# Kernel optimization log

Measured on AMD Instinct MI355X. Metric: run time of the kernel, lower is better.

## Reference

```python
import jax, jax.numpy as jnp
import numpy as np
from jax import lax

HEADS = 4
DSTATE = 8
DHALF = 64
DTRANK = 8
GRID_SIZE = 5
SPLINE_ORDER = 3


def _ln(x, g, b, eps=1e-5):
    mu = x.mean(-1, keepdims=True)
    v = ((x - mu) ** 2).mean(-1, keepdims=True)
    return (x - mu) / jnp.sqrt(v + eps) * g + b


def _make_grid(in_f):
    h = 2.0 / GRID_SIZE
    g = jnp.arange(-SPLINE_ORDER, GRID_SIZE + SPLINE_ORDER + 1, dtype=jnp.float32) * h - 1.0
    return jnp.tile(g[None, :], (in_f, 1))  # (in, grid+2k+1)


def _b_splines(x, grid):
    # x: (batch, in); grid: (in, G+2k+1) -> (batch, in, G+k)
    xe = x[:, :, None]
    bases = ((xe >= grid[:, :-1]) & (xe < grid[:, 1:])).astype(x.dtype)
    for k in range(1, SPLINE_ORDER + 1):
        bases = ((xe - grid[:, :-(k + 1)]) / (grid[:, k:-1] - grid[:, :-(k + 1)])) * bases[:, :, :-1] \
              + ((grid[:, k + 1:] - xe) / (grid[:, k + 1:] - grid[:, 1:-k])) * bases[:, :, 1:]
    return bases


def _kan_layer(x, bw, sw, sc, grid):
    base = jax.nn.silu(x) @ bw.T
    bs = _b_splines(x, grid)
    return base + jnp.einsum('bic,oic->bo', bs, sw * sc[:, :, None])


def _fkan(x, ng, nb, bw0, sw0, sc0, bw1, sw1, sc1):
    B, N, C = x.shape
    xf = _ln(x, ng, nb).reshape(B * N, C)
    h = _kan_layer(xf, bw0, sw0, sc0, _make_grid(C))
    y = _kan_layer(h, bw1, sw1, sc1, _make_grid(bw0.shape[0]))
    return y.reshape(B, N, C)


def _conv1x1(x, w, b):
    return jnp.einsum('bchw,oc->bohw', x, w[:, :, 0, 0]) + b[None, :, None, None]


def _dwconv2d(x, w, b):
    y = lax.conv_general_dilated(x, w, (1, 1), 'SAME', feature_group_count=x.shape[1],
                                 dimension_numbers=('NCHW', 'OIHW', 'NCHW'))
    return y + b[None, :, None, None]


def _dwconv1d(x, w):
    return lax.conv_general_dilated(x, w, (1,), 'SAME', feature_group_count=x.shape[1],
                                    dimension_numbers=('NCH', 'OIH', 'NCH'))


def _attention(x, temp, qkv_w, qkv_b, dw_w, dw_b, po_w, po_b):
    b, c, h, w = x.shape
    qkv = _dwconv2d(_conv1x1(x, qkv_w, qkv_b), dw_w, dw_b)
    q, k, v = jnp.split(qkv, 3, axis=1)
    rs = lambda t: t.reshape(b, HEADS, c // HEADS, h * w)
    q, k, v = rs(q), rs(k), rs(v)
    q = q / jnp.maximum(jnp.linalg.norm(q, axis=-1, keepdims=True), 1e-12)
    k = k / jnp.maximum(jnp.linalg.norm(k, axis=-1, keepdims=True), 1e-12)
    attn = jax.nn.softmax(jnp.einsum('bhcn,bhdn->bhcd', q, k) * temp, axis=-1)
    out = jnp.einsum('bhcd,bhdn->bhcn', attn, v).reshape(b, c, h, w)
    return _conv1x1(out, po_w, po_b)


def _mamba(x, in_w, xp_w, dt_w, dt_b, A_log, Dp, out_w, cx_w, cz_w):
    B, L, C = x.shape
    xz = x @ in_w.T                       # (B, L, d_inner)
    xc, zc = jnp.split(xz, 2, axis=-1)    # each (B, L, DHALF)
    xl = jax.nn.silu(_dwconv1d(xc.transpose(0, 2, 1), cx_w)).transpose(0, 2, 1)
    zl = jax.nn.silu(_dwconv1d(zc.transpose(0, 2, 1), cz_w)).transpose(0, 2, 1)
    x_dbl = xl @ xp_w.T                   # (B, L, dt_rank + 2*d_state)
    dt, Bm, Cm = jnp.split(x_dbl, [DTRANK, DTRANK + DSTATE], axis=-1)
    delta = jax.nn.softplus(dt @ dt_w.T + dt_b)   # (B, L, DHALF)
    A = -jnp.exp(A_log)                   # (DHALF, DSTATE)
    dA = jnp.exp(jnp.einsum('bld,dn->bldn', delta, A))
    dBu = delta[..., None] * Bm[:, :, None, :] * xl[..., None]

    def step(hst, inp):
        dA_t, dBu_t, C_t = inp
        hst = dA_t * hst + dBu_t
        return hst, jnp.einsum('bdn,bn->bd', hst, C_t)

    h0 = jnp.zeros((B, DHALF, DSTATE), x.dtype)
    _, ys = lax.scan(step, h0, (dA.transpose(1, 0, 2, 3), dBu.transpose(1, 0, 2, 3), Cm.transpose(1, 0, 2)))
    y = ys.transpose(1, 0, 2) + xl * Dp
    return jnp.concatenate([y, zl], axis=-1) @ out_w.T


def _forward(x5d, ln1_g, ln1_b, ln2_g, ln2_b, ln3_g, ln3_b, ln4_g, ln4_b,
             attn_temp, attn_qkv_w, attn_qkv_b, attn_dw_w, attn_dw_b, attn_po_w, attn_po_b,
             ffn1_ng, ffn1_nb, ffn1_bw0, ffn1_sw0, ffn1_sc0, ffn1_bw1, ffn1_sw1, ffn1_sc1,
             ffn2_ng, ffn2_nb, ffn2_bw0, ffn2_sw0, ffn2_sc0, ffn2_bw1, ffn2_sw1, ffn2_sc1,
             in_proj_w, x_proj_w, dt_proj_w, dt_proj_b, A_log, D_param, out_proj_w, conv_x_w, conv_z_w):
    B, C, Dd, H, W = x5d.shape
    N = Dd * H * W
    Hs = int(np.sqrt(N))
    x = x5d.reshape(B, C, N).transpose(0, 2, 1)   # (B, N, C)
    t2d = _ln(x, ln1_g, ln1_b).transpose(0, 2, 1).reshape(B, C, Hs, Hs)
    a = _attention(t2d, attn_temp, attn_qkv_w, attn_qkv_b, attn_dw_w, attn_dw_b, attn_po_w, attn_po_b)
    t = x + a.reshape(B, C, N).transpose(0, 2, 1)
    u = _fkan(_ln(t, ln2_g, ln2_b), ffn1_ng, ffn1_nb, ffn1_bw0, ffn1_sw0, ffn1_sc0, ffn1_bw1, ffn1_sw1, ffn1_sc1) + t
    x_tr = x + u
    m = _mamba(_ln(x_tr, ln3_g, ln3_b), in_proj_w, x_proj_w, dt_proj_w, dt_proj_b, A_log, D_param, out_proj_w, conv_x_w, conv_z_w) + x_tr
    n = _fkan(_ln(m, ln4_g, ln4_b), ffn2_ng, ffn2_nb, ffn2_bw0, ffn2_sw0, ffn2_sc0, ffn2_bw1, ffn2_sw1, ffn2_sc1) + m
    out = x_tr + n
    return out.transpose(0, 2, 1).reshape(B, C, Dd, H, W)


def setup_inputs():
    key = jax.random.key(0)
    ks = iter(jax.random.split(key, 48))
    f32 = jnp.float32

    def rn(shape, s=0.05):
        return jax.random.normal(next(ks), shape, f32) * s

    B, C, Dd, H, W = 2, 128, 1, 96, 96
    MLP = 512
    d = {}
    d['x5d'] = jax.random.normal(next(ks), (B, C, Dd, H, W), f32)
    for nm in ('ln1', 'ln2', 'ln3', 'ln4'):
        d[nm + '_g'] = jnp.ones((C,), f32)
        d[nm + '_b'] = jnp.zeros((C,), f32)
    d['attn_temp'] = jnp.ones((HEADS, 1, 1), f32)
    d['attn_qkv_w'] = rn((3 * C, C, 1, 1)); d['attn_qkv_b'] = jnp.zeros((3 * C,), f32)
    d['attn_dw_w'] = rn((3 * C, 1, 3, 3), 0.2); d['attn_dw_b'] = jnp.zeros((3 * C,), f32)
    d['attn_po_w'] = rn((C, C, 1, 1)); d['attn_po_b'] = jnp.zeros((C,), f32)
    for p in ('ffn1', 'ffn2'):
        d[p + '_ng'] = jnp.ones((C,), f32); d[p + '_nb'] = jnp.zeros((C,), f32)
        d[p + '_bw0'] = rn((MLP, C)); d[p + '_sw0'] = rn((MLP, C, GRID_SIZE + SPLINE_ORDER), 0.02); d[p + '_sc0'] = jnp.ones((MLP, C), f32)
        d[p + '_bw1'] = rn((C, MLP)); d[p + '_sw1'] = rn((C, MLP, GRID_SIZE + SPLINE_ORDER), 0.02); d[p + '_sc1'] = jnp.ones((C, MLP), f32)
    d['in_proj_w'] = rn((C, C))
    d['x_proj_w'] = rn((DTRANK + 2 * DSTATE, DHALF))
    std = DTRANK ** -0.5
    d['dt_proj_w'] = jax.random.uniform(next(ks), (DHALF, DTRANK), f32, -std, std)
    dt = jnp.exp(jax.random.uniform(next(ks), (DHALF,), f32) * (np.log(0.1) - np.log(0.001)) + np.log(0.001))
    dt = jnp.clip(dt, 1e-4, None)
    d['dt_proj_b'] = dt + jnp.log(-jnp.expm1(-dt))
    d['A_log'] = jnp.log(jnp.tile(jnp.arange(1, DSTATE + 1, dtype=f32)[None, :], (DHALF, 1)))
    d['D_param'] = jnp.ones((DHALF,), f32)
    d['out_proj_w'] = rn((C, C))
    d['conv_x_w'] = rn((DHALF, 1, 3), 0.2)
    d['conv_z_w'] = rn((DHALF, 1, 3), 0.2)
    return d


def reference(x5d, ln1_g, ln1_b, ln2_g, ln2_b, ln3_g, ln3_b, ln4_g, ln4_b,
              attn_temp, attn_qkv_w, attn_qkv_b, attn_dw_w, attn_dw_b, attn_po_w, attn_po_b,
              ffn1_ng, ffn1_nb, ffn1_bw0, ffn1_sw0, ffn1_sc0, ffn1_bw1, ffn1_sw1, ffn1_sc1,
              ffn2_ng, ffn2_nb, ffn2_bw0, ffn2_sw0, ffn2_sc0, ffn2_bw1, ffn2_sw1, ffn2_sc1,
              in_proj_w, x_proj_w, dt_proj_w, dt_proj_b, A_log, D_param, out_proj_w, conv_x_w, conv_z_w):
    return _forward(x5d, ln1_g, ln1_b, ln2_g, ln2_b, ln3_g, ln3_b, ln4_g, ln4_b,
                    attn_temp, attn_qkv_w, attn_qkv_b, attn_dw_w, attn_dw_b, attn_po_w, attn_po_b,
                    ffn1_ng, ffn1_nb, ffn1_bw0, ffn1_sw0, ffn1_sc0, ffn1_bw1, ffn1_sw1, ffn1_sc1,
                    ffn2_ng, ffn2_nb, ffn2_bw0, ffn2_sw0, ffn2_sc0, ffn2_bw1, ffn2_sw1, ffn2_sc1,
                    in_proj_w, x_proj_w, dt_proj_w, dt_proj_b, A_log, D_param, out_proj_w, conv_x_w, conv_z_w)
```

## Files before the change

### kernel.cpp

```cpp
#include <hip/hip_runtime.h>

typedef unsigned short u16;
typedef __attribute__((ext_vector_type(8))) short bh8;
typedef __attribute__((ext_vector_type(4))) float f4;

#define DI __device__ __forceinline__

DI u16 f2bf(float f){ unsigned u=__float_as_uint(f); u += 0x7fffu + ((u>>16)&1u); return (u16)(u>>16); }
DI float bf2f(u16 u){ return __uint_as_float(((unsigned)u)<<16); }
DI float silu_f(float x){ return x/(1.f+__expf(-x)); }

DI void gld16(const u16* g, u16* l){
  __builtin_amdgcn_global_load_lds((const __attribute__((address_space(1))) void*)g,
                                   (__attribute__((address_space(3))) void*)l, 16, 0, 0);
}

DI void bspline8(float x, float* v){
  float u = x*2.5f + 5.5f;
  #pragma unroll
  for (int j=0;j<8;j++){
    float a  = fabsf(u - (float)(j+2));
    float t1 = fmaxf(2.f-a, 0.f);
    float t2 = fmaxf(1.f-a, 0.f);
    v[j] = t1*t1*t1*(1.f/6.f) - t2*t2*t2*(2.f/3.f);
  }
}

template<int KAN_H, bool OUT_BF16>
__global__ __launch_bounds__(256, 6)
void gemm64(const void* __restrict__ Asrc, const u16* __restrict__ Bt,
            void* __restrict__ Cout, int M, int N, int K, int ktiles_per_z,
            int split, const float* __restrict__ bias, const float* __restrict__ R1)
{
  __shared__ __align__(128) u16 smem[12296];
  u16* const sB = smem;
  u16* const sA = smem + 8192;
  const int m0 = blockIdx.y * 64;
  const int n0 = blockIdx.x * 128;
  const int ktiles = K >> 6;
  int kt0 = blockIdx.z * ktiles_per_z;
  int kt1 = kt0 + ktiles_per_z; if (kt1 > ktiles) kt1 = ktiles;
  const int t = threadIdx.x;
  const int wave = t >> 6, lane = t & 63;
  const int lr = lane & 15, lq = lane >> 4;
  const int lr8 = lane >> 3, lc8 = lane & 7;
  const int swz8 = lc8 ^ lr8;
  f4 acc[4][2];
  f4 z4 = {0.f,0.f,0.f,0.f};
  #pragma unroll
  for (int i=0;i<4;i++){ acc[i][0]=z4; acc[i][1]=z4; }

  for (int kt = kt0; kt < kt1; ++kt) {
    int k0 = kt << 6;
    {
      const u16* Bp = Bt + (size_t)n0 * K + k0;
      #pragma unroll
      for (int it=0; it<4; ++it) {
        int r = it*32 + wave*8;
        gld16(Bp + (size_t)(r + lr8) * K + swz8*8, &sB[r*64]);
      }
    }
    if (KAN_H == 0) {
      const u16* Ap = (const u16*)Asrc + (size_t)m0 * K + k0;
      #pragma unroll
      for (int it=0; it<2; ++it) {
        int r = it*32 + wave*8;
        gld16(Ap + (size_t)(r + lr8) * K + swz8*8, &sA[r*64]);
      }
    } else {
      const u16* hsrc = (const u16*)Asrc;
      if (k0 < KAN_H) {
        #pragma unroll
        for (int it=0; it<2; ++it) {
          int chunk = t + it*256;
          int r = chunk >> 3, ck = chunk & 7;
          const u16* src = hsrc + (size_t)(m0+r)*KAN_H + k0 + ck*8;
          ushort4 a = *(const ushort4*)src;
          ushort4 b2 = *(const ushort4*)(src+4);
          alignas(16) u16 o[8];
          o[0]=f2bf(silu_f(bf2f(a.x))); o[1]=f2bf(silu_f(bf2f(a.y)));
          o[2]=f2bf(silu_f(bf2f(a.z))); o[3]=f2bf(silu_f(bf2f(a.w)));
          o[4]=f2bf(silu_f(bf2f(b2.x))); o[5]=f2bf(silu_f(bf2f(b2.y)));
          o[6]=f2bf(silu_f(bf2f(b2.z))); o[7]=f2bf(silu_f(bf2f(b2.w)));
          *(float4*)(&sA[r*64 + (ck ^ (r&7))*8]) = *(const float4*)o;
        }
      } else {
        int i0 = (k0 - KAN_H) >> 3;
        const float4 zf4 = make_float4(0.f,0.f,0.f,0.f);
        #pragma unroll
        for (int it=0; it<2; ++it) {
          int pair = t + it*256;
          int r = pair >> 3, ii = pair & 7;
          int base = r*64 + (ii ^ (r&7))*8;
          *(float4*)(&sA[base]) = zf4;
          float x = bf2f(hsrc[(size_t)(m0+r)*KAN_H + i0 + ii]);
          float u = x*2.5f + 5.5f;
          bool valid = (u >= 0.f) & (u < 11.f);
          float uc = fminf(fmaxf(u, 0.f), 10.999f);
          int m = (int)uc;
          float tt = uc - (float)m;
          float omt = 1.f - tt, t2 = tt*tt, t3 = t2*tt;
          float w0 = omt*omt*omt*(1.f/6.f);
          float w3 = t3*(1.f/6.f);
          float w1 = 0.5f*t3 - t2 + (2.f/3.f);
          float w2 = 1.f - w0 - w1 - w3;
          float ws[4] = {w0, w1, w2, w3};
          int c0 = m - 3;
          #pragma unroll
          for (int j=0;j<4;j++){
            int c = c0 + j;
            bool ok = valid & ((unsigned)c < 8u);
            int off = ok ? (base + c) : 4096;
            sA[off] = f2bf(ws[j]);
          }
        }
      }
    }
    __syncthreads();
    #pragma unroll
    for (int kk=0; kk<64; kk+=32) {
      const int c0k = kk >> 3;
      bh8 af[4], bfr[2];
      #pragma unroll
      for (int i=0;i<4;i++) {
        int row = i*16 + lr;
        af[i] = *(const bh8*)(&sA[row*64 + ((c0k+lq) ^ (row&7))*8]);
      }
      #pragma unroll
      for (int j=0;j<2;j++) {
        int row = wave*32 + j*16 + lr;
        bfr[j] = *(const bh8*)(&sB[row*64 + ((c0k+lq) ^ (row&7))*8]);
      }
      #pragma unroll
      for (int i=0;i<4;i++)
        #pragma unroll
        for (int j=0;j<2;j++)
          acc[i][j] = __builtin_amdgcn_mfma_f32_16x16x32_bf16(af[i], bfr[j], acc[i][j], 0, 0, 0);
    }
    __syncthreads();
  }
  if (OUT_BF16) {
    u16* Cb = (u16*)Cout;
    #pragma unroll
    for (int i=0;i<4;i++) {
      #pragma unroll
      for (int j=0;j<2;j++) {
        int col = wave*32 + j*16 + lr;
        float bv = bias ? bias[n0 + col] : 0.f;
        #pragma unroll
        for (int r4=0;r4<4;r4++) {
          int row = i*16 + lq*4 + r4;
          smem[row*136 + col] = f2bf(acc[i][j][r4] + bv);
        }
      }
    }
    __syncthreads();
    #pragma unroll
    for (int it=0; it<4; ++it) {
      int idx = t + it*256;
      int row = idx >> 4, seg = idx & 15;
      *(float4*)(Cb + (size_t)(m0+row)*N + n0 + seg*8) =
          *(const float4*)&smem[row*136 + seg*8];
    }
  } else {
    float* Cf = (float*)Cout;
    if (split) Cf += (size_t)blockIdx.z * M * N;
    #pragma unroll
    for (int i=0;i<4;i++) {
      int row = m0 + i*16 + lq*4;
      #pragma unroll
      for (int j=0;j<2;j++) {
        int col = n0 + wave*32 + j*16 + lr;
        float bv = bias ? bias[col] : 0.f;
        #pragma unroll
        for (int r4=0;r4<4;r4++) {
          size_t idx = (size_t)(row + r4) * N + col;
          float v = acc[i][j][r4] + bv;
          if (R1) v += R1[idx];
          Cf[idx] = v;
        }
      }
    }
  }
}

__global__ __launch_bounds__(256) void k_ln1_trans(const float* __restrict__ x5d,
    float* __restrict__ x_t, u16* __restrict__ ln1_t,
    const float* __restrict__ g, const float* __restrict__ bv)
{
  __shared__ float tile[128*65];
  __shared__ float red_s[256], red_q[256];
  __shared__ float st_mu[64], st_rs[64];
  int b = blockIdx.y, n0 = blockIdx.x * 64;
  int j = threadIdx.x & 63, part = threadIdx.x >> 6;
  for (int cc=0; cc<32; ++cc) {
    int c = part*32 + cc;
    tile[c*65 + j] = x5d[((size_t)b*128 + c)*9216 + n0 + j];
  }
  __syncthreads();
  float s=0.f, s2=0.f;
  for (int cc=0; cc<32; ++cc) {
    float v = tile[(part*32+cc)*65 + j];
    s += v; s2 += v*v;
  }
  red_s[threadIdx.x]=s; red_q[threadIdx.x]=s2;
  __syncthreads();
  if (threadIdx.x < 64) {
    int jj = threadIdx.x;
    float ts = red_s[jj]+red_s[jj+64]+red_s[jj+128]+red_s[jj+192];
    float tq = red_q[jj]+red_q[jj+64]+red_q[jj+128]+red_q[jj+192];
    float mu = ts*(1.f/128.f);
    st_mu[jj]=mu;
    st_rs[jj]=rsqrtf(tq*(1.f/128.f) - mu*mu + 1e-5f);
  }
  __syncthreads();
  for (int it=0; it<32; ++it) {
    int idx = threadIdx.x + it*256;
    int tok = idx >> 7, c = idx & 127;
    float v = tile[c*65 + tok];
    size_t a = ((size_t)b*9216 + n0 + tok)*128 + c;
    x_t[a] = v;
    ln1_t[a] = f2bf((v - st_mu[tok])*st_rs[tok]*g[c] + bv[c]);
  }
}

__global__ void k_ln_double_expand(const float* __restrict__ in, u16* __restrict__ A1,
    const float* __restrict__ g1, const float* __restrict__ b1,
    const float* __restrict__ g2, const float* __restrict__ b2)
{
  int tok = blockIdx.x*4 + (threadIdx.x>>6);
  int lane = threadIdx.x & 63;
  const float* row = in + (size_t)tok*128;
  float v0=row[lane], v1=row[lane+64];
  float s=v0+v1, s2=v0*v0+v1*v1;
  #pragma unroll
  for (int o=1;o<64;o<<=1){ s += __shfl_xor(s,o); s2 += __shfl_xor(s2,o); }
  float mu=s*(1.f/128.f);
  float rs=rsqrtf(s2*(1.f/128.f)-mu*mu+1e-5f);
  float y0=(v0-mu)*rs*g1[lane]+b1[lane];
  float y1=(v1-mu)*rs*g1[lane+64]+b1[lane+64];
  s=y0+y1; s2=y0*y0+y1*y1;
  #pragma unroll
  for (int o=1;o<64;o<<=1){ s += __shfl_xor(s,o); s2 += __shfl_xor(s2,o); }
  mu=s*(1.f/128.f);
  rs=rsqrtf(s2*(1.f/128.f)-mu*mu+1e-5f);
  y0=(y0-mu)*rs*g2[lane]+b2[lane];
  y1=(y1-mu)*rs*g2[lane+64]+b2[lane+64];
  u16* arow = A1 + (size_t)tok*1152;
  arow[lane]    = f2bf(silu_f(y0));
  arow[lane+64] = f2bf(silu_f(y1));
  float w[8]; alignas(16) u16 o8[8];
  bspline8(y0, w);
  #pragma unroll
  for (int j=0;j<8;j++) o8[j]=f2bf(w[j]);
  *(float4*)(&arow[128 + lane*8]) = *(const float4*)o8;
  bspline8(y1, w);
  #pragma unroll
  for (int j=0;j<8;j++) o8[j]=f2bf(w[j]);
  *(float4*)(&arow[128 + (lane+64)*8]) = *(const float4*)o8;
}

__global__ __launch_bounds__(256) void k_dwconv(const u16* __restrict__ qkv_t,
    u16* __restrict__ qkvd, const float* __restrict__ dw_w, const float* __restrict__ dw_b)
{
  __shared__ float lt[100*68];
  int tile = blockIdx.x; int th=(tile/12)*8, tw=(tile%12)*8;
  int cg = blockIdx.y, b = blockIdx.z;
  int t = threadIdx.x;
  for (int pp=0; pp<7; ++pp) {
    int pos = pp*16 + (t>>4);
    if (pos < 100) {
      int ih = th + pos/10 - 1, iw = tw + pos%10 - 1;
      int c4 = (t & 15)*4;
      float4 v = make_float4(0.f,0.f,0.f,0.f);
      if (ih>=0 && ih<96 && iw>=0 && iw<96) {
        ushort4 raw = *(const ushort4*)&qkv_t[(((size_t)b*9216) + ih*96 + iw)*384 + cg*64 + c4];
        v = make_float4(bf2f(raw.x), bf2f(raw.y), bf2f(raw.z), bf2f(raw.w));
      }
      *(float4*)&lt[pos*68 + c4] = v;
    }
  }
  __syncthreads();
  int ch = t & 63, gch = cg*64 + ch;
  float w[9];
  #pragma unroll
  for (int k=0;k<9;k++) w[k]=dw_w[gch*9+k];
  float bias = dw_b[gch];
  for (int pp=0; pp<16; ++pp) {
    int pos = (t>>6) + pp*4;
    int oh = pos>>3, ow = pos&7;
    float acc = bias;
    #pragma unroll
    for (int di=0; di<3; ++di)
      #pragma unroll
      for (int dj=0; dj<3; ++dj)
        acc += lt[((oh+di)*10 + ow+dj)*68 + ch] * w[di*3+dj];
    qkvd[(((size_t)b*9216) + (th+oh)*96 + tw+ow)*384 + gch] = f2bf(acc);
  }
}

__global__ void k_normsum(const u16* __restrict__ qkvd, float* __restrict__ ss)
{
  int b = blockIdx.y, n0 = blockIdx.x*128;
  int c = threadIdx.x;
  float acc=0.f;
  for (int i=0;i<128;++i){
    float v = bf2f(qkvd[((size_t)b*9216 + n0+i)*384 + c]);
    acc += v*v;
  }
  atomicAdd(&ss[b*256 + c], acc);
}

__global__ __launch_bounds__(256) void k_qk(const u16* __restrict__ qkvd,
    const float* __restrict__ ss, float* __restrict__ S)
{
  __shared__ float ql[128][32];
  __shared__ float kl[128][32];
  int nc=blockIdx.x, h=blockIdx.y, b=blockIdx.z;
  int t = threadIdx.x;
  int r = t>>1, half = t&1;
  size_t rowa = ((size_t)b*9216 + nc*128 + r)*384 + (half?128:0) + h*32;
  #pragma unroll
  for (int cc=0; cc<32; ++cc) {
    float v = bf2f(qkvd[rowa + cc]);
    if (half) kl[r][cc]=v; else ql[r][cc]=v;
  }
  __syncthreads();
  int i0 = (t>>4)*2, j0 = (t&15)*2;
  float a00=0.f,a01=0.f,a10=0.f,a11=0.f;
  for (int n=0;n<128;++n){
    float2 qv = *(const float2*)&ql[n][i0];
    float2 kv = *(const float2*)&kl[n][j0];
    a00 += qv.x*kv.x; a01 += qv.x*kv.y;
    a10 += qv.y*kv.x; a11 += qv.y*kv.y;
  }
  const float* ssb = ss + b*256;
  float rq0 = 1.f/fmaxf(sqrtf(ssb[h*32+i0]),1e-12f);
  float rq1 = 1.f/fmaxf(sqrtf(ssb[h*32+i0+1]),1e-12f);
  float rk0 = 1.f/fmaxf(sqrtf(ssb[128+h*32+j0]),1e-12f);
  float rk1 = 1.f/fmaxf(sqrtf(ssb[128+h*32+j0+1]),1e-12f);
  float* Sp = S + ((size_t)(b*4+h))*1024;
  atomicAdd(&Sp[i0*32+j0],     a00*rq0*rk0);
  atomicAdd(&Sp[i0*32+j0+1],   a01*rq0*rk1);
  atomicAdd(&Sp[(i0+1)*32+j0], a10*rq1*rk0);
  atomicAdd(&Sp[(i0+1)*32+j0+1], a11*rq1*rk1);
}

__global__ void k_softmax(const float* __restrict__ S, float* __restrict__ attnP,
                          const float* __restrict__ temp)
{
  int bh = blockIdx.x; int h = bh & 3;
  int i = threadIdx.x;
  const float* row = S + (size_t)bh*1024 + i*32;
  float tp = temp[h];
  float vals[32]; float mx = -1e30f;
  #pragma unroll
  for (int j=0;j<32;++j){ float v=row[j]*tp; vals[j]=v; mx=fmaxf(mx,v); }
  float sum=0.f;
  #pragma unroll
  for (int j=0;j<32;++j){ vals[j]=__expf(vals[j]-mx); sum+=vals[j]; }
  float inv=1.f/sum;
  float* out = attnP + (size_t)bh*1024 + i*32;
  #pragma unroll
  for (int j=0;j<32;++j) out[j]=vals[j]*inv;
}

__global__ __launch_bounds__(256) void k_av(const u16* __restrict__ qkvd,
    const float* __restrict__ attnP, u16* __restrict__ attnout)
{
  __shared__ float at[1024];
  int b=blockIdx.z, h=blockIdx.y;
  int n = blockIdx.x*256 + threadIdx.x;
  #pragma unroll
  for (int it=0;it<4;++it)
    at[threadIdx.x + it*256] = attnP[((size_t)(b*4+h))*1024 + threadIdx.x + it*256];
  __syncthreads();
  const u16* vrow = &qkvd[((size_t)b*9216 + n)*384 + 256 + h*32];
  float acc[32];
  #pragma unroll
  for (int i=0;i<32;++i) acc[i]=0.f;
  #pragma unroll 4
  for (int j=0;j<32;++j){
    float vj = bf2f(vrow[j]);
    #pragma unroll
    for (int i=0;i<32;++i) acc[i] += at[i*32+j]*vj;
  }
  u16* orow = &attnout[((size_t)b*9216 + n)*128 + h*32];
  #pragma unroll
  for (int i=0;i<32;++i) orow[i] = f2bf(acc[i]);
}

__global__ void k_reduce4(const float4* __restrict__ P, const float4* __restrict__ R1,
                          const float4* __restrict__ R2, float4* __restrict__ o, int n4)
{
  int i = blockIdx.x*256 + threadIdx.x;
  if (i<n4){
    float4 a=P[i], b=P[i+n4], c=P[i+2*n4], d=P[i+3*n4], r=R1[i], s=R2[i];
    o[i]=make_float4(a.x+b.x+c.x+d.x+r.x+s.x, a.y+b.y+c.y+d.y+r.y+s.y,
                     a.z+b.z+c.z+d.z+r.z+s.z, a.w+b.w+c.w+d.w+r.w+s.w);
  }
}

__global__ void k_reduce4_ln(const float4* __restrict__ P, const float4* __restrict__ R1,
    const float4* __restrict__ R2, float4* __restrict__ xtr, u16* __restrict__ xm,
    const float* __restrict__ g, const float* __restrict__ bv, int n4)
{
  int i = blockIdx.x*256 + threadIdx.x;
  int q = i & 31;
  float4 a=P[i], b=P[i+n4], c=P[i+2*n4], d=P[i+3*n4], r=R1[i], s=R2[i];
  float4 v=make_float4(a.x+b.x+c.x+d.x+r.x+s.x, a.y+b.y+c.y+d.y+r.y+s.y,
                       a.z+b.z+c.z+d.z+r.z+s.z, a.w+b.w+c.w+d.w+r.w+s.w);
  xtr[i]=v;
  float s1 = v.x+v.y+v.z+v.w;
  float s2 = v.x*v.x+v.y*v.y+v.z*v.z+v.w*v.w;
  #pragma unroll
  for (int o=1;o<32;o<<=1){ s1 += __shfl_xor(s1,o); s2 += __shfl_xor(s2,o); }
  float mu = s1*(1.f/128.f);
  float rs = rsqrtf(s2*(1.f/128.f)-mu*mu+1e-5f);
  float4 g4 = *(const float4*)(g + q*4);
  float4 b4 = *(const float4*)(bv + q*4);
  ushort4 o4;
  o4.x = f2bf((v.x-mu)*rs*g4.x + b4.x);
  o4.y = f2bf((v.y-mu)*rs*g4.y + b4.y);
  o4.z = f2bf((v.z-mu)*rs*g4.z + b4.z);
  o4.w = f2bf((v.w-mu)*rs*g4.w + b4.w);
  ((ushort4*)xm)[i] = o4;
}

__global__ void k_prep(const float* __restrict__ qkv_w, const float* __restrict__ po_w,
    const float* __restrict__ in_w, const float* __restrict__ out_w,
    const float* __restrict__ A_log, u16* __restrict__ qkvw_bf, u16* __restrict__ pow_bf,
    u16* __restrict__ inw_bf, u16* __restrict__ outw_bf, float* __restrict__ Aneg,
    float* __restrict__ zbuf, int nz)
{
  int i = blockIdx.x*256 + threadIdx.x;
  if (i < 49152) { qkvw_bf[i] = f2bf(qkv_w[i]); return; }
  i -= 49152;
  if (i < 16384) { pow_bf[i] = f2bf(po_w[i]); return; }
  i -= 16384;
  if (i < 16384) { inw_bf[i] = f2bf(in_w[i]); return; }
  i -= 16384;
  if (i < 16384) { outw_bf[i] = f2bf(out_w[i]); return; }
  i -= 16384;
  if (i < 512) { Aneg[i] = -__expf(A_log[i]); return; }
  i -= 512;
  if (i < nz) zbuf[i] = 0.f;
}

__global__ __launch_bounds__(256) void k_mamba_pre(const float* __restrict__ xz,
    float* __restrict__ xl, float* __restrict__ delta,
    float* __restrict__ Bm, float* __restrict__ Cm, u16* __restrict__ A_out,
    const float* __restrict__ cxw, const float* __restrict__ czw,
    const float* __restrict__ xpw, const float* __restrict__ dtw, const float* __restrict__ dtb)
{
  __shared__ float xls[4][64];
  __shared__ float xds[4][24];
  int w = threadIdx.x>>6;
  int tok = blockIdx.x*4 + w;
  int lane = threadIdx.x & 63;
  int l = tok % 9216;
  size_t base = (size_t)tok*128;
  float xm1 = (l>0)?     xz[base-128+lane]    : 0.f;
  float x0  =            xz[base+lane];
  float xp1 = (l<9215)?  xz[base+128+lane]    : 0.f;
  float zm1 = (l>0)?     xz[base-128+64+lane] : 0.f;
  float z0  =            xz[base+64+lane];
  float zp1 = (l<9215)?  xz[base+128+64+lane] : 0.f;
  float xc = silu_f(cxw[lane*3]*xm1 + cxw[lane*3+1]*x0 + cxw[lane*3+2]*xp1);
  float zc = silu_f(czw[lane*3]*zm1 + czw[lane*3+1]*z0 + czw[lane*3+2]*zp1);
  xl[(size_t)tok*64+lane] = xc;
  A_out[(size_t)tok*128 + 64 + lane] = f2bf(zc);
  xls[w][lane] = xc;
  __syncthreads();
  if (lane < 24) {
    float s=0.f;
    #pragma unroll 8
    for (int c=0;c<64;++c) s += xls[w][c]*xpw[lane*64+c];
    xds[w][lane]=s;
  }
  __syncthreads();
  float dacc = dtb[lane];
  #pragma unroll
  for (int r=0;r<8;++r) dacc += xds[w][r]*dtw[lane*8+r];
  delta[(size_t)tok*64+lane] = (dacc>20.f)? dacc : log1pf(__expf(dacc));
  if (lane<8)       Bm[(size_t)tok*8+lane]   = xds[w][8+lane];
  else if (lane<16) Cm[(size_t)tok*8+lane-8] = xds[w][16+lane-8];
}

__global__ __launch_bounds__(512) void k_scan1(const float* __restrict__ delta,
    const float* __restrict__ Bm, const float* __restrict__ xl,
    const float* __restrict__ Aneg, float* __restrict__ cP, float* __restrict__ cS)
{
  int b=blockIdx.y, ch=blockIdx.x;
  int t=threadIdx.x; int d=t>>3, n=t&7;
  float An = Aneg[d*8+n];
  float P=1.f, S=0.f;
  int l0 = ch*96;
  #pragma unroll 8
  for (int i=0;i<96;++i){
    size_t s = (size_t)b*9216 + l0+i;
    float del = delta[s*64+d];
    float a = __expf(del*An);
    float dbu = del * Bm[s*8+n] * xl[s*64+d];
    P *= a; S = fmaf(a,S,dbu);
  }
  size_t o = ((size_t)(b*96+ch))*512 + t;
  cP[o]=P; cS[o]=S;
}

__global__ __launch_bounds__(512) void k_scan2(const float* __restrict__ cP,
    const float* __restrict__ cS, float* __restrict__ cI)
{
  int b=blockIdx.x; int t=threadIdx.x;
  float carry=0.f;
  #pragma unroll 4
  for (int c=0;c<96;++c){
    size_t o = ((size_t)(b*96+c))*512 + t;
    cI[o]=carry;
    carry = fmaf(cP[o], carry, cS[o]);
  }
}

__global__ __launch_bounds__(512) void k_scan3(const float* __restrict__ delta,
    const float* __restrict__ Bm, const float* __restrict__ Cm,
    const float* __restrict__ xl, const float* __restrict__ Aneg,
    const float* __restrict__ Dp, const float* __restrict__ cI, u16* __restrict__ A_out)
{
  int b=blockIdx.y, ch=blockIdx.x;
  int t=threadIdx.x; int d=t>>3, n=t&7;
  float An = Aneg[d*8+n];
  float h = cI[((size_t)(b*96+ch))*512 + t];
  float Dd = Dp[d];
  int l0 = ch*96;
  #pragma unroll 4
  for (int i=0;i<96;++i){
    size_t s = (size_t)b*9216 + l0+i;
    float del = delta[s*64+d];
    float a = __expf(del*An);
    float xv = xl[s*64+d];
    h = fmaf(a, h, del * Bm[s*8+n] * xv);
    float contrib = h * Cm[s*8+n];
    contrib += __shfl_xor(contrib,1);
    contrib += __shfl_xor(contrib,2);
    contrib += __shfl_xor(contrib,4);
    if (n==0) A_out[s*128 + d] = f2bf(contrib + xv*Dd);
  }
}

__global__ __launch_bounds__(256) void k_transpose_out(const float* __restrict__ sfin,
                                                       float* __restrict__ out)
{
  __shared__ float tile[128*65];
  int b=blockIdx.y, n0=blockIdx.x*64;
  for (int it=0;it<32;++it){
    int idx = threadIdx.x + it*256;
    int tok = idx>>7, c = idx&127;
    tile[c*65+tok] = sfin[((size_t)b*9216 + n0+tok)*128 + c];
  }
  __syncthreads();
  int j = threadIdx.x & 63, part = threadIdx.x>>6;
  for (int cc=0;cc<32;++cc){
    int c = part*32+cc;
    out[((size_t)b*128 + c)*9216 + n0 + j] = tile[c*65 + j];
  }
}

__global__ void k_pack_w1t(const float* __restrict__ bw0, const float* __restrict__ sw0,
                           const float* __restrict__ sc0, u16* __restrict__ W1t)
{
  int idx = blockIdx.x*256 + threadIdx.x;
  if (idx >= 512*1152) return;
  int o = idx/1152, k = idx%1152;
  float v;
  if (k < 128) v = bw0[o*128+k];
  else { int i=(k-128)>>3, c=(k-128)&7; v = sw0[(o*128+i)*8+c]*sc0[o*128+i]; }
  W1t[idx]=f2bf(v);
}
__global__ void k_pack_w2t(const float* __restrict__ bw1, const float* __restrict__ sw1,
                           const float* __restrict__ sc1, u16* __restrict__ W2t)
{
  int idx = blockIdx.x*256 + threadIdx.x;
  if (idx >= 128*4608) return;
  int o = idx/4608, k = idx%4608;
  float v;
  if (k < 512) v = bw1[o*512+k];
  else { int i=(k-512)>>3, c=(k-512)&7; v = sw1[(o*512+i)*8+c]*sc1[o*512+i]; }
  W2t[idx]=f2bf(v);
}

extern "C" void kernel_launch(void* const* d_in, const int* in_sizes, int n_in,
                              void* d_out, int out_size, void* d_ws, size_t ws_size,
                              hipStream_t stream)
{
  (void)in_sizes; (void)n_in; (void)out_size; (void)ws_size;
  const float* x5d   =(const float*)d_in[0];
  const float* ln1_g =(const float*)d_in[1];
  const float* ln1_b =(const float*)d_in[2];
  const float* ln2_g =(const float*)d_in[3];
  const float* ln2_b =(const float*)d_in[4];
  const float* ln3_g =(const float*)d_in[5];
  const float* ln3_b =(const float*)d_in[6];
  const float* ln4_g =(const float*)d_in[7];
  const float* ln4_b =(const float*)d_in[8];
  const float* temp  =(const float*)d_in[9];
  const float* qkv_w =(const float*)d_in[10];
  const float* qkv_b =(const float*)d_in[11];
  const float* dw_w  =(const float*)d_in[12];
  const float* dw_b  =(const float*)d_in[13];
  const float* po_w  =(const float*)d_in[14];
  const float* po_b  =(const float*)d_in[15];
  const float* f1_ng =(const float*)d_in[16];
  const float* f1_nb =(const float*)d_in[17];
  const float* f1_bw0=(const float*)d_in[18];
  const float* f1_sw0=(const float*)d_in[19];
  const float* f1_sc0=(const float*)d_in[20];
  const float* f1_bw1=(const float*)d_in[21];
  const float* f1_sw1=(const float*)d_in[22];
  const float* f1_sc1=(const float*)d_in[23];
  const float* f2_ng =(const float*)d_in[24];
  const float* f2_nb =(const float*)d_in[25];
  const float* f2_bw0=(const float*)d_in[26];
  const float* f2_sw0=(const float*)d_in[27];
  const float* f2_sc0=(const float*)d_in[28];
  const float* f2_bw1=(const float*)d_in[29];
  const float* f2_sw1=(const float*)d_in[30];
  const float* f2_sc1=(const float*)d_in[31];
  const float* in_w  =(const float*)d_in[32];
  const float* xp_w  =(const float*)d_in[33];
  const float* dt_w  =(const float*)d_in[34];
  const float* dt_b  =(const float*)d_in[35];
  const float* A_log =(const float*)d_in[36];
  const float* Dp    =(const float*)d_in[37];
  const float* out_w =(const float*)d_in[38];
  const float* cx_w  =(const float*)d_in[39];
  const float* cz_w  =(const float*)d_in[40];
  float* out = (float*)d_out;

  const size_t T = 18432;
  char* wsb = (char*)d_ws;
  size_t off = 0;
  auto alloc = [&](size_t bytes)->void* {
    void* p = wsb + off; off += (bytes + 255) & ~(size_t)255; return p;
  };
  float* x_t    = (float*)alloc(T*128*4);
  char*  scrA   = (char*) alloc(38*1024*1024);
  float* ssS    = (float*)alloc((512+8192+8192)*4);
  float* t_t    = (float*)alloc(T*128*4);
  u16*   A1     = (u16*)  alloc(T*1152*2);
  u16*   hbuf   = (u16*)  alloc(T*512*2);
  float* xtr    = (float*)alloc(T*128*4);
  u16*   xm     = (u16*)  alloc(T*128*2);
  float* xl     = (float*)alloc(T*64*4);
  float* delta  = (float*)alloc(T*64*4);
  float* Bm     = (float*)alloc(T*8*4);
  float* Cm     = (float*)alloc(T*8*4);
  u16*   A_out  = (u16*)  alloc(T*128*2);
  float* cP     = (float*)alloc(2*96*512*4);
  float* cS     = (float*)alloc(2*96*512*4);
  float* cI     = (float*)alloc(2*96*512*4);
  float* sfin   = (float*)alloc(T*128*4);
  u16* qkvw_bf  = (u16*)alloc(384*128*2);
  u16* pow_bf   = (u16*)alloc(128*128*2);
  u16* inw_bf   = (u16*)alloc(128*128*2);
  u16* outw_bf  = (u16*)alloc(128*128*2);
  u16* W1t_a    = (u16*)alloc(512*1152*2);
  u16* W2t_a    = (u16*)alloc(128*4608*2);
  u16* W1t_b    = (u16*)alloc(512*1152*2);
  u16* W2t_b    = (u16*)alloc(128*4608*2);
  float* Aneg   = (float*)alloc(512*4);
  float* ss = ssS;
  float* S  = ssS + 512;
  float* attnP = ssS + 512 + 8192;
  u16*   ln1_t  = (u16*)(scrA);
  u16*   qkv_tb = (u16*)(scrA + 4718592);
  u16*   qkvd   = (u16*)(scrA + 4718592 + 14155776);
  u16*   attnout= (u16*)(scrA + 4718592 + 2*14155776);
  float* part   = (float*)scrA;
  float* xz     = (float*)scrA;
  float* m_t    = t_t;

  k_pack_w1t<<<2304,256,0,stream>>>(f1_bw0, f1_sw0, f1_sc0, W1t_a);
  k_pack_w1t<<<2304,256,0,stream>>>(f2_bw0, f2_sw0, f2_sc0, W1t_b);
  k_pack_w2t<<<2304,256,0,stream>>>(f1_bw1, f1_sw1, f1_sc1, W2t_a);
  k_pack_w2t<<<2304,256,0,stream>>>(f2_bw1, f2_sw1, f2_sc1, W2t_b);
  k_prep<<<420,256,0,stream>>>(qkv_w, po_w, in_w, out_w, A_log,
      qkvw_bf, pow_bf, inw_bf, outw_bf, Aneg, ssS, 512+8192);

  k_ln1_trans<<<dim3(144,2),256,0,stream>>>(x5d, x_t, ln1_t, ln1_g, ln1_b);
  gemm64<0,true><<<dim3(3,288,1),256,0,stream>>>(ln1_t, qkvw_bf, qkv_tb,
      18432, 384, 128, 2, 0, qkv_b, nullptr);
  k_dwconv<<<dim3(144,6,2),256,0,stream>>>(qkv_tb, qkvd, dw_w, dw_b);
  k_normsum<<<dim3(72,2),256,0,stream>>>(qkvd, ss);
  k_qk<<<dim3(72,4,2),256,0,stream>>>(qkvd, ss, S);
  k_softmax<<<8,32,0,stream>>>(S, attnP, temp);
  k_av<<<dim3(36,4,2),256,0,stream>>>(qkvd, attnP, attnout);
  gemm64<0,false><<<dim3(1,288,1),256,0,stream>>>(attnout, pow_bf, t_t,
      18432, 128, 128, 2, 0, po_b, x_t);

  k_ln_double_expand<<<4608,256,0,stream>>>(t_t, A1, ln2_g, ln2_b, f1_ng, f1_nb);
  gemm64<0,true><<<dim3(4,288,1),256,0,stream>>>(A1, W1t_a, hbuf,
      18432, 512, 1152, 18, 0, nullptr, nullptr);
  gemm64<512,false><<<dim3(1,288,4),256,0,stream>>>(hbuf, W2t_a, part,
      18432, 128, 4608, 18, 1, nullptr, nullptr);
  k_reduce4_ln<<<2304,256,0,stream>>>((const float4*)part, (const float4*)t_t,
      (const float4*)x_t, (float4*)xtr, xm, ln3_g, ln3_b, (int)(T*128/4));

  gemm64<0,false><<<dim3(1,288,1),256,0,stream>>>(xm, inw_bf, xz,
      18432, 128, 128, 2, 0, nullptr, nullptr);
  k_mamba_pre<<<4608,256,0,stream>>>(xz, xl, delta, Bm, Cm, A_out,
      cx_w, cz_w, xp_w, dt_w, dt_b);
  k_scan1<<<dim3(96,2),512,0,stream>>>(delta, Bm, xl, Aneg, cP, cS);
  k_scan2<<<2,512,0,stream>>>(cP, cS, cI);
  k_scan3<<<dim3(96,2),512,0,stream>>>(delta, Bm, Cm, xl, Aneg, Dp, cI, A_out);
  gemm64<0,false><<<dim3(1,288,1),256,0,stream>>>(A_out, outw_bf, m_t,
      18432, 128, 128, 2, 0, nullptr, xtr);

  k_ln_double_expand<<<4608,256,0,stream>>>(m_t, A1, ln4_g, ln4_b, f2_ng, f2_nb);
  gemm64<0,true><<<dim3(4,288,1),256,0,stream>>>(A1, W1t_b, hbuf,
      18432, 512, 1152, 18, 0, nullptr, nullptr);
  gemm64<512,false><<<dim3(1,288,4),256,0,stream>>>(hbuf, W2t_b, part,
      18432, 128, 4608, 18, 1, nullptr, nullptr);
  k_reduce4<<<2304,256,0,stream>>>((const float4*)part, (const float4*)m_t,
      (const float4*)xtr, (float4*)sfin, (int)(T*128/4));

  k_transpose_out<<<dim3(144,2),256,0,stream>>>(sfin, out);
}
```

Baseline: 535.1 us.

## Fuse norm-sum into dwconv, bf16 split-K partials, merge reduce+transpose and weight packing

Accumulates the q/k squared norms inside the depthwise conv kernel, so the separate norm-sum pass that re-read qkvd is no longer needed. The split-K GEMM partials for the second KAN layer are now written as bf16, which halves partial-buffer traffic at the cost of rounding before the reduction. The final residual reduction is fused with the output transpose, which removes the intermediate fp32 buffer. The weight-packing kernels are merged into one launch, and GEMM launch bounds are relaxed from 6 to 4 waves per SIMD.

Result: faster. 513.8 us (-4.0%).

```diff
diff --git a/kernel.cpp b/kernel.cpp
--- a/kernel.cpp
+++ b/kernel.cpp
@@ -27,7 +27,7 @@
 }
 
 template<int KAN_H, bool OUT_BF16>
-__global__ __launch_bounds__(256, 6)
+__global__ __launch_bounds__(256, 4)
 void gemm64(const void* __restrict__ Asrc, const u16* __restrict__ Bt,
             void* __restrict__ Cout, int M, int N, int K, int ktiles_per_z,
             int split, const float* __restrict__ bias, const float* __restrict__ R1)
@@ -141,6 +141,7 @@
   }
   if (OUT_BF16) {
     u16* Cb = (u16*)Cout;
+    if (split) Cb += (size_t)blockIdx.z * M * N;
     #pragma unroll
     for (int i=0;i<4;i++) {
       #pragma unroll
@@ -261,7 +262,8 @@
 }
 
 __global__ __launch_bounds__(256) void k_dwconv(const u16* __restrict__ qkv_t,
-    u16* __restrict__ qkvd, const float* __restrict__ dw_w, const float* __restrict__ dw_b)
+    u16* __restrict__ qkvd, const float* __restrict__ dw_w, const float* __restrict__ dw_b,
+    float* __restrict__ ss)
 {
   __shared__ float lt[100*68];
   int tile = blockIdx.x; int th=(tile/12)*8, tw=(tile%12)*8;
@@ -286,6 +288,7 @@
   #pragma unroll
   for (int k=0;k<9;k++) w[k]=dw_w[gch*9+k];
   float bias = dw_b[gch];
+  float sq = 0.f;
   for (int pp=0; pp<16; ++pp) {
     int pos = (t>>6) + pp*4;
     int oh = pos>>3, ow = pos&7;
@@ -295,20 +298,18 @@
       #pragma unroll
       for (int dj=0; dj<3; ++dj)
         acc += lt[((oh+di)*10 + ow+dj)*68 + ch] * w[di*3+dj];
+    sq += acc*acc;
     qkvd[(((size_t)b*9216) + (th+oh)*96 + tw+ow)*384 + gch] = f2bf(acc);
   }
-}
-
-__global__ void k_normsum(const u16* __restrict__ qkvd, float* __restrict__ ss)
-{
-  int b = blockIdx.y, n0 = blockIdx.x*128;
-  int c = threadIdx.x;
-  float acc=0.f;
-  for (int i=0;i<128;++i){
-    float v = bf2f(qkvd[((size_t)b*9216 + n0+i)*384 + c]);
-    acc += v*v;
-  }
-  atomicAdd(&ss[b*256 + c], acc);
+  if (cg < 4) {
+    __syncthreads();
+    lt[(t>>6)*64 + ch] = sq;
+    __syncthreads();
+    if (t < 64) {
+      float s = lt[t] + lt[64+t] + lt[128+t] + lt[192+t];
+      atomicAdd(&ss[b*256 + cg*64 + t], s);
+    }
+  }
 }
 
 __global__ __launch_bounds__(256) void k_qk(const u16* __restrict__ qkvd,
@@ -390,26 +391,18 @@
   for (int i=0;i<32;++i) orow[i] = f2bf(acc[i]);
 }
 
-__global__ void k_reduce4(const float4* __restrict__ P, const float4* __restrict__ R1,
-                          const float4* __restrict__ R2, float4* __restrict__ o, int n4)
-{
-  int i = blockIdx.x*256 + threadIdx.x;
-  if (i<n4){
-    float4 a=P[i], b=P[i+n4], c=P[i+2*n4], d=P[i+3*n4], r=R1[i], s=R2[i];
-    o[i]=make_float4(a.x+b.x+c.x+d.x+r.x+s.x, a.y+b.y+c.y+d.y+r.y+s.y,
-                     a.z+b.z+c.z+d.z+r.z+s.z, a.w+b.w+c.w+d.w+r.w+s.w);
-  }
-}
-
-__global__ void k_reduce4_ln(const float4* __restrict__ P, const float4* __restrict__ R1,
+__global__ void k_reduce4_ln(const ushort4* __restrict__ P, const float4* __restrict__ R1,
     const float4* __restrict__ R2, float4* __restrict__ xtr, u16* __restrict__ xm,
     const float* __restrict__ g, const float* __restrict__ bv, int n4)
 {
   int i = blockIdx.x*256 + threadIdx.x;
   int q = i & 31;
-  float4 a=P[i], b=P[i+n4], c=P[i+2*n4], d=P[i+3*n4], r=R1[i], s=R2[i];
-  float4 v=make_float4(a.x+b.x+c.x+d.x+r.x+s.x, a.y+b.y+c.y+d.y+r.y+s.y,
-                       a.z+b.z+c.z+d.z+r.z+s.z, a.w+b.w+c.w+d.w+r.w+s.w);
+  ushort4 a=P[i], b=P[i+n4], c=P[i+2*n4], d=P[i+3*n4];
+  float4 r=R1[i], s=R2[i];
+  float4 v=make_float4(bf2f(a.x)+bf2f(b.x)+bf2f(c.x)+bf2f(d.x)+r.x+s.x,
+                       bf2f(a.y)+bf2f(b.y)+bf2f(c.y)+bf2f(d.y)+r.y+s.y,
+                       bf2f(a.z)+bf2f(b.z)+bf2f(c.z)+bf2f(d.z)+r.z+s.z,
+                       bf2f(a.w)+bf2f(b.w)+bf2f(c.w)+bf2f(d.w)+r.w+s.w);
   xtr[i]=v;
   float s1 = v.x+v.y+v.z+v.w;
   float s2 = v.x*v.x+v.y*v.y+v.z*v.z+v.w*v.w;
@@ -427,13 +420,75 @@
   ((ushort4*)xm)[i] = o4;
 }
 
-__global__ void k_prep(const float* __restrict__ qkv_w, const float* __restrict__ po_w,
+__global__ __launch_bounds__(256) void k_reduce4_trans(const ushort4* __restrict__ P,
+    const float4* __restrict__ R1, const float4* __restrict__ R2,
+    float* __restrict__ out, int n4)
+{
+  __shared__ float tile[128*65];
+  int b=blockIdx.y, n0=blockIdx.x*64;
+  for (int it=0; it<8; ++it) {
+    int idx = threadIdx.x + it*256;
+    int tok = idx >> 5, c4 = idx & 31;
+    int gi = (b*9216 + n0 + tok)*32 + c4;
+    ushort4 a=P[gi], bb=P[gi+n4], c=P[gi+2*n4], d=P[gi+3*n4];
+    float4 r=R1[gi], s=R2[gi];
+    tile[(c4*4+0)*65+tok] = bf2f(a.x)+bf2f(bb.x)+bf2f(c.x)+bf2f(d.x)+r.x+s.x;
+    tile[(c4*4+1)*65+tok] = bf2f(a.y)+bf2f(bb.y)+bf2f(c.y)+bf2f(d.y)+r.y+s.y;
+    tile[(c4*4+2)*65+tok] = bf2f(a.z)+bf2f(bb.z)+bf2f(c.z)+bf2f(d.z)+r.z+s.z;
+    tile[(c4*4+3)*65+tok] = bf2f(a.w)+bf2f(bb.w)+bf2f(c.w)+bf2f(d.w)+r.w+s.w;
+  }
+  __syncthreads();
+  int j = threadIdx.x & 63, part = threadIdx.x>>6;
+  for (int cc=0;cc<32;++cc){
+    int c = part*32+cc;
+    out[((size_t)b*128 + c)*9216 + n0 + j] = tile[c*65 + j];
+  }
+}
+
+__global__ void k_pack_all(
+    const float* __restrict__ f1_bw0, const float* __restrict__ f1_sw0, const float* __restrict__ f1_sc0,
+    const float* __restrict__ f2_bw0, const float* __restrict__ f2_sw0, const float* __restrict__ f2_sc0,
+    const float* __restrict__ f1_bw1, const float* __restrict__ f1_sw1, const float* __restrict__ f1_sc1,
+    const float* __restrict__ f2_bw1, const float* __restrict__ f2_sw1, const float* __restrict__ f2_sc1,
+    const float* __restrict__ qkv_w, const float* __restrict__ po_w,
     const float* __restrict__ in_w, const float* __restrict__ out_w,
-    const float* __restrict__ A_log, u16* __restrict__ qkvw_bf, u16* __restrict__ pow_bf,
-    u16* __restrict__ inw_bf, u16* __restrict__ outw_bf, float* __restrict__ Aneg,
-    float* __restrict__ zbuf, int nz)
+    const float* __restrict__ A_log,
+    u16* __restrict__ W1t_a, u16* __restrict__ W1t_b,
+    u16* __restrict__ W2t_a, u16* __restrict__ W2t_b,
+    u16* __restrict__ qkvw_bf, u16* __restrict__ pow_bf,
+    u16* __restrict__ inw_bf, u16* __restrict__ outw_bf,
+    float* __restrict__ Aneg, float* __restrict__ zbuf, int nz)
 {
   int i = blockIdx.x*256 + threadIdx.x;
+  const int NW1 = 512*1152, NW2 = 128*4608;
+  if (i < NW1) {
+    int o = i/1152, k = i%1152; float v;
+    if (k < 128) v = f1_bw0[o*128+k];
+    else { int f=(k-128)>>3, c=(k-128)&7; v = f1_sw0[(o*128+f)*8+c]*f1_sc0[o*128+f]; }
+    W1t_a[i]=f2bf(v); return;
+  }
+  i -= NW1;
+  if (i < NW1) {
+    int o = i/1152, k = i%1152; float v;
+    if (k < 128) v = f2_bw0[o*128+k];
+    else { int f=(k-128)>>3, c=(k-128)&7; v = f2_sw0[(o*128+f)*8+c]*f2_sc0[o*128+f]; }
+    W1t_b[i]=f2bf(v); return;
+  }
+  i -= NW1;
+  if (i < NW2) {
+    int o = i/4608, k = i%4608; float v;
+    if (k < 512) v = f1_bw1[o*512+k];
+    else { int f=(k-512)>>3, c=(k-512)&7; v = f1_sw1[(o*512+f)*8+c]*f1_sc1[o*512+f]; }
+    W2t_a[i]=f2bf(v); return;
+  }
+  i -= NW2;
+  if (i < NW2) {
+    int o = i/4608, k = i%4608; float v;
+    if (k < 512) v = f2_bw1[o*512+k];
+    else { int f=(k-512)>>3, c=(k-512)&7; v = f2_sw1[(o*512+f)*8+c]*f2_sc1[o*512+f]; }
+    W2t_b[i]=f2bf(v); return;
+  }
+  i -= NW2;
   if (i < 49152) { qkvw_bf[i] = f2bf(qkv_w[i]); return; }
   i -= 49152;
   if (i < 16384) { pow_bf[i] = f2bf(po_w[i]); return; }
@@ -545,47 +600,6 @@
     contrib += __shfl_xor(contrib,4);
     if (n==0) A_out[s*128 + d] = f2bf(contrib + xv*Dd);
   }
-}
-
-__global__ __launch_bounds__(256) void k_transpose_out(const float* __restrict__ sfin,
-                                                       float* __restrict__ out)
-{
-  __shared__ float tile[128*65];
-  int b=blockIdx.y, n0=blockIdx.x*64;
-  for (int it=0;it<32;++it){
-    int idx = threadIdx.x + it*256;
-    int tok = idx>>7, c = idx&127;
-    tile[c*65+tok] = sfin[((size_t)b*9216 + n0+tok)*128 + c];
-  }
-  __syncthreads();
-  int j = threadIdx.x & 63, part = threadIdx.x>>6;
-  for (int cc=0;cc<32;++cc){
-    int c = part*32+cc;
-    out[((size_t)b*128 + c)*9216 + n0 + j] = tile[c*65 + j];
-  }
-}
-
-__global__ void k_pack_w1t(const float* __restrict__ bw0, const float* __restrict__ sw0,
-                           const float* __restrict__ sc0, u16* __restrict__ W1t)
-{
-  int idx = blockIdx.x*256 + threadIdx.x;
-  if (idx >= 512*1152) return;
-  int o = idx/1152, k = idx%1152;
-  float v;
-  if (k < 128) v = bw0[o*128+k];
-  else { int i=(k-128)>>3, c=(k-128)&7; v = sw0[(o*128+i)*8+c]*sc0[o*128+i]; }
-  W1t[idx]=f2bf(v);
-}
-__global__ void k_pack_w2t(const float* __restrict__ bw1, const float* __restrict__ sw1,
-                           const float* __restrict__ sc1, u16* __restrict__ W2t)
-{
-  int idx = blockIdx.x*256 + threadIdx.x;
-  if (idx >= 128*4608) return;
-  int o = idx/4608, k = idx%4608;
-  float v;
-  if (k < 512) v = bw1[o*512+k];
-  else { int i=(k-512)>>3, c=(k-512)&7; v = sw1[(o*512+i)*8+c]*sc1[o*512+i]; }
-  W2t[idx]=f2bf(v);
 }
 
 extern "C" void kernel_launch(void* const* d_in, const int* in_sizes, int n_in,
@@ -658,7 +672,6 @@
   float* cP     = (float*)alloc(2*96*512*4);
   float* cS     = (float*)alloc(2*96*512*4);
   float* cI     = (float*)alloc(2*96*512*4);
-  float* sfin   = (float*)alloc(T*128*4);
   u16* qkvw_bf  = (u16*)alloc(384*128*2);
   u16* pow_bf   = (u16*)alloc(128*128*2);
   u16* inw_bf   = (u16*)alloc(128*128*2);
@@ -675,22 +688,22 @@
   u16*   qkv_tb = (u16*)(scrA + 4718592);
   u16*   qkvd   = (u16*)(scrA + 4718592 + 14155776);
   u16*   attnout= (u16*)(scrA + 4718592 + 2*14155776);
-  float* part   = (float*)scrA;
+  u16*   partb  = (u16*)scrA;
   float* xz     = (float*)scrA;
   float* m_t    = t_t;
-
-  k_pack_w1t<<<2304,256,0,stream>>>(f1_bw0, f1_sw0, f1_sc0, W1t_a);
-  k_pack_w1t<<<2304,256,0,stream>>>(f2_bw0, f2_sw0, f2_sc0, W1t_b);
-  k_pack_w2t<<<2304,256,0,stream>>>(f1_bw1, f1_sw1, f1_sc1, W2t_a);
-  k_pack_w2t<<<2304,256,0,stream>>>(f2_bw1, f2_sw1, f2_sc1, W2t_b);
-  k_prep<<<420,256,0,stream>>>(qkv_w, po_w, in_w, out_w, A_log,
+  const int n4 = (int)(T*128/4);
+
+  k_pack_all<<<9636,256,0,stream>>>(
+      f1_bw0,f1_sw0,f1_sc0, f2_bw0,f2_sw0,f2_sc0,
+      f1_bw1,f1_sw1,f1_sc1, f2_bw1,f2_sw1,f2_sc1,
+      qkv_w, po_w, in_w, out_w, A_log,
+      W1t_a, W1t_b, W2t_a, W2t_b,
       qkvw_bf, pow_bf, inw_bf, outw_bf, Aneg, ssS, 512+8192);
 
   k_ln1_trans<<<dim3(144,2),256,0,stream>>>(x5d, x_t, ln1_t, ln1_g, ln1_b);
   gemm64<0,true><<<dim3(3,288,1),256,0,stream>>>(ln1_t, qkvw_bf, qkv_tb,
       18432, 384, 128, 2, 0, qkv_b, nullptr);
-  k_dwconv<<<dim3(144,6,2),256,0,stream>>>(qkv_tb, qkvd, dw_w, dw_b);
-  k_normsum<<<dim3(72,2),256,0,stream>>>(qkvd, ss);
+  k_dwconv<<<dim3(144,6,2),256,0,stream>>>(qkv_tb, qkvd, dw_w, dw_b, ss);
   k_qk<<<dim3(72,4,2),256,0,stream>>>(qkvd, ss, S);
   k_softmax<<<8,32,0,stream>>>(S, attnP, temp);
   k_av<<<dim3(36,4,2),256,0,stream>>>(qkvd, attnP, attnout);
@@ -700,10 +713,10 @@
   k_ln_double_expand<<<4608,256,0,stream>>>(t_t, A1, ln2_g, ln2_b, f1_ng, f1_nb);
   gemm64<0,true><<<dim3(4,288,1),256,0,stream>>>(A1, W1t_a, hbuf,
       18432, 512, 1152, 18, 0, nullptr, nullptr);
-  gemm64<512,false><<<dim3(1,288,4),256,0,stream>>>(hbuf, W2t_a, part,
+  gemm64<512,true><<<dim3(1,288,4),256,0,stream>>>(hbuf, W2t_a, partb,
       18432, 128, 4608, 18, 1, nullptr, nullptr);
-  k_reduce4_ln<<<2304,256,0,stream>>>((const float4*)part, (const float4*)t_t,
-      (const float4*)x_t, (float4*)xtr, xm, ln3_g, ln3_b, (int)(T*128/4));
+  k_reduce4_ln<<<2304,256,0,stream>>>((const ushort4*)partb, (const float4*)t_t,
+      (const float4*)x_t, (float4*)xtr, xm, ln3_g, ln3_b, n4);
 
   gemm64<0,false><<<dim3(1,288,1),256,0,stream>>>(xm, inw_bf, xz,
       18432, 128, 128, 2, 0, nullptr, nullptr);
@@ -718,10 +731,8 @@
   k_ln_double_expand<<<4608,256,0,stream>>>(m_t, A1, ln4_g, ln4_b, f2_ng, f2_nb);
   gemm64<0,true><<<dim3(4,288,1),256,0,stream>>>(A1, W1t_b, hbuf,
       18432, 512, 1152, 18, 0, nullptr, nullptr);
-  gemm64<512,false><<<dim3(1,288,4),256,0,stream>>>(hbuf, W2t_b, part,
+  gemm64<512,true><<<dim3(1,288,4),256,0,stream>>>(hbuf, W2t_b, partb,
       18432, 128, 4608, 18, 1, nullptr, nullptr);
-  k_reduce4<<<2304,256,0,stream>>>((const float4*)part, (const float4*)m_t,
-      (const float4*)xtr, (float4*)sfin, (int)(T*128/4));
-
-  k_transpose_out<<<dim3(144,2),256,0,stream>>>(sfin, out);
-}
+  k_reduce4_trans<<<dim3(144,2),256,0,stream>>>((const ushort4*)partb,
+      (const float4*)m_t, (const float4*)xtr, out, n4);
+}
```
